# Kernel tuning notes

Hardware: AMD Instinct MI355X
Metric: run time of the kernel (lower is better)

The kernel has to match this reference:

```python
import jax, jax.numpy as jnp
import numpy as np


def _glorot(key, shape):
    fan_in, fan_out = shape[0], shape[1]
    lim = np.sqrt(6.0 / (fan_in + fan_out))
    return jax.random.uniform(key, shape, jnp.float32, -lim, lim)


def setup_inputs() -> dict:
    key = jax.random.key(0)
    ks = jax.random.split(key, 32)
    B, NR, NT = 16384, 64, 128
    inp = {
        "tier0_features": jax.random.normal(ks[0], (B, 44), jnp.float32),
        "robot_features": jax.random.normal(ks[1], (B, NR, 6), jnp.float32),
        "track_features": jax.random.normal(ks[2], (B, NT, 7), jnp.float32),
        # robot SetEncoder: 6 -> 64 -> 64 -> 32
        "rw1": _glorot(ks[3], (6, 64)),  "rb1": jnp.zeros((64,), jnp.float32),
        "rw2": _glorot(ks[4], (64, 64)), "rb2": jnp.zeros((64,), jnp.float32),
        "rw3": _glorot(ks[5], (64, 32)), "rb3": jnp.zeros((32,), jnp.float32),
        # track SetEncoder: 7 -> 64 -> 64 -> 32
        "tw1": _glorot(ks[6], (7, 64)),  "tb1": jnp.zeros((64,), jnp.float32),
        "tw2": _glorot(ks[7], (64, 64)), "tb2": jnp.zeros((64,), jnp.float32),
        "tw3": _glorot(ks[8], (64, 32)), "tb3": jnp.zeros((32,), jnp.float32),
        # head MLP: 108 -> 128 -> 128 -> 64 -> 1
        "mw1": _glorot(ks[9], (108, 128)),  "mb1": jnp.zeros((128,), jnp.float32),
        "mw2": _glorot(ks[10], (128, 128)), "mb2": jnp.zeros((128,), jnp.float32),
        "mw3": _glorot(ks[11], (128, 64)),  "mb3": jnp.zeros((64,), jnp.float32),
        "mw4": _glorot(ks[12], (64, 1)),    "mb4": jnp.zeros((1,), jnp.float32),
    }
    return inp


def _set_encode(x, w1, b1, w2, b2, w3, b3):
    # x: [B, N, d_in] -> pooled [B, 32]; mask=None path: mean+max over set dim
    h = jax.nn.relu(jnp.einsum('bnd,dh->bnh', x, w1) + b1)
    h = jax.nn.relu(jnp.einsum('bnh,hk->bnk', h, w2) + b2)
    e = jnp.einsum('bnk,ko->bno', h, w3) + b3
    return (e.mean(axis=1) + e.max(axis=1)) * 0.5


def reference(tier0_features, robot_features, track_features,
              rw1, rb1, rw2, rb2, rw3, rb3,
              tw1, tb1, tw2, tb2, tw3, tb3,
              mw1, mb1, mw2, mb2, mw3, mb3, mw4, mb4):
    robot_emb = _set_encode(robot_features, rw1, rb1, rw2, rb2, rw3, rb3)  # [B,32]
    track_emb = _set_encode(track_features, tw1, tb1, tw2, tb2, tw3, tb3)  # [B,32]
    c = jnp.concatenate([tier0_features, robot_emb, track_emb], axis=1)    # [B,108]
    h = jax.nn.relu(c @ mw1 + mb1)
    h = jax.nn.relu(h @ mw2 + mb2)
    h = jax.nn.relu(h @ mw3 + mb3)
    return (h @ mw4 + mb4).squeeze(-1)  # [B]
```

## Files before the change

### kernel.cpp

```cpp
#include <hip/hip_runtime.h>
#include <hip/hip_bf16.h>

#define DEV_INLINE __device__ __forceinline__
#define MEM_FENCE asm volatile("" ::: "memory")

typedef __bf16 bf16x8 __attribute__((ext_vector_type(8)));
typedef float  floatx4 __attribute__((ext_vector_type(4)));

DEV_INLINE bf16x8 ld_frag(const __bf16* p) {
    union { uint4 u; bf16x8 v; } t;
    t.u = *(const uint4*)p;
    return t.v;
}
DEV_INLINE bf16x8 pack_relu2(floatx4 a, floatx4 b) {
    float2 p0 = {fmaxf(a[0], 0.0f), fmaxf(a[1], 0.0f)};
    float2 p1 = {fmaxf(a[2], 0.0f), fmaxf(a[3], 0.0f)};
    float2 p2 = {fmaxf(b[0], 0.0f), fmaxf(b[1], 0.0f)};
    float2 p3 = {fmaxf(b[2], 0.0f), fmaxf(b[3], 0.0f)};
    union { __hip_bfloat162 h[4]; bf16x8 v; } t;
    t.h[0] = __float22bfloat162_rn(p0);
    t.h[1] = __float22bfloat162_rn(p1);
    t.h[2] = __float22bfloat162_rn(p2);
    t.h[3] = __float22bfloat162_rn(p3);
    return t.v;
}
DEV_INLINE floatx4 vmax4(floatx4 a, floatx4 b) {
    floatx4 r;
#pragma unroll
    for (int i = 0; i < 4; ++i) r[i] = fmaxf(a[i], b[i]);
    return r;
}

template<int N, int Kp, int Ks>
DEV_INLINE void tp(__bf16* dst, const float* __restrict__ src, int idx0, int stride) {
    for (int e = idx0; e < N * Kp; e += stride) {
        int n = e / Kp, k = e - n * Kp;
        dst[e] = (k < Ks) ? (__bf16)src[k * N + n] : (__bf16)0.0f;
    }
}
template<int N, int K>
DEV_INLINE void tp_perm(__bf16* dst, const float* __restrict__ src, int idx0, int stride) {
    for (int e = idx0; e < N * K; e += stride) {
        int n = e / K, kh = e - n * K;
        int qd = (kh >> 3) & 3, kq = kh >> 5, j = kh & 7;
        int c = (2 * kq + (j >> 2)) * 16 + qd * 4 + (j & 3);
        dst[e] = (__bf16)src[c * N + n];
    }
}

__global__ __launch_bounds__(256)
void prep_kernel(const float* __restrict__ rw1, const float* __restrict__ rw2,
                 const float* __restrict__ rw3,
                 const float* __restrict__ tw1, const float* __restrict__ tw2,
                 const float* __restrict__ tw3,
                 const float* __restrict__ mw1, const float* __restrict__ mw2,
                 const float* __restrict__ mw3, __bf16* __restrict__ wb)
{
    int i0 = blockIdx.x * 256 + threadIdx.x;
    int st = gridDim.x * 256;
    tp     < 64,  32,   6>(wb + 0,     rw1, i0, st);
    tp_perm< 64,  64>     (wb + 2048,  rw2, i0, st);
    tp_perm< 32,  64>     (wb + 6144,  rw3, i0, st);
    tp     < 64,  32,   7>(wb + 8192,  tw1, i0, st);
    tp_perm< 64,  64>     (wb + 10240, tw2, i0, st);
    tp_perm< 32,  64>     (wb + 14336, tw3, i0, st);
    tp     <128, 128, 108>(wb + 16384, mw1, i0, st);
    tp_perm<128, 128>     (wb + 32768, mw2, i0, st);
    tp_perm< 64, 128>     (wb + 49152, mw3, i0, st);
}

struct __align__(16) EncSmem {
    float  e3s[64 * 36];
    float  e3m[64 * 36];
    __bf16 w1[64 * 40];
    __bf16 w2[64 * 72];
    __bf16 w3[32 * 72];
    float  bs[160];
};

template<int DIN, int S>
DEV_INLINE void enc_body(EncSmem& sm, const float* __restrict__ X,
                         const __bf16* __restrict__ wenc,
                         const float* __restrict__ b1, const float* __restrict__ b2,
                         const float* __restrict__ b3,
                         __bf16* __restrict__ out, int bid)
{
    constexpr int NB = 128 / S;
    const int tid = threadIdx.x;
    const int w   = tid >> 6;
    const int l64 = tid & 63;
    const int ln  = l64 & 15;
    const int qd  = l64 >> 4;
    float* pool = (float*)sm.w1;

    {
        const uint4* wsrc = (const uint4*)wenc;
        { int i = tid, r = i >> 2, c = i & 3;  *(uint4*)&sm.w1[r * 40 + c * 8] = wsrc[i]; }
        for (int i = tid; i < 512; i += 256) {
            int r = i >> 3, c = i & 7;  *(uint4*)&sm.w2[r * 72 + c * 8] = wsrc[256 + i];
        }
        { int i = tid, r = i >> 3, c = i & 7;  *(uint4*)&sm.w3[r * 72 + c * 8] = wsrc[768 + i]; }
        if (tid < 160)
            sm.bs[tid] = (tid < 64) ? b1[tid]
                       : (tid < 128) ? b2[tid - 64] : b3[tid - 128];
    }
    __syncthreads();

    bf16x8 xb[2];
#pragma unroll
    for (int t = 0; t < 2; ++t) {
        bf16x8 v;
#pragma unroll
        for (int j = 0; j < 8; ++j) v[j] = (__bf16)0.0f;
        if (qd == 0) {
            const int row = (2 * w + t) * 16 + ln;
            const float* xp = X + ((size_t)bid * 128 + row) * DIN;
#pragma unroll
            for (int j = 0; j < DIN; ++j) v[j] = (__bf16)xp[j];
        }
        xb[t] = v;
    }
    floatx4 a1[2][4];
#pragma unroll
    for (int mt = 0; mt < 4; ++mt) {
        bf16x8 af = ld_frag(&sm.w1[(mt * 16 + ln) * 40 + qd * 8]);
        float4 bv = *(const float4*)&sm.bs[mt * 16 + qd * 4];
#pragma unroll
        for (int t = 0; t < 2; ++t) {
            floatx4 acc = (floatx4){bv.x, bv.y, bv.z, bv.w};
            a1[t][mt] = __builtin_amdgcn_mfma_f32_16x16x32_bf16(af, xb[t], acc, 0, 0, 0);
        }
    }
    bf16x8 f1[2][2];
#pragma unroll
    for (int t = 0; t < 2; ++t)
#pragma unroll
        for (int kq = 0; kq < 2; ++kq)
            f1[t][kq] = pack_relu2(a1[t][2 * kq], a1[t][2 * kq + 1]);

    floatx4 a2[2][4];
#pragma unroll
    for (int mt = 0; mt < 4; ++mt) {
        bf16x8 a0 = ld_frag(&sm.w2[(mt * 16 + ln) * 72 + qd * 8]);
        bf16x8 a1f = ld_frag(&sm.w2[(mt * 16 + ln) * 72 + 32 + qd * 8]);
        float4 bv = *(const float4*)&sm.bs[64 + mt * 16 + qd * 4];
#pragma unroll
        for (int t = 0; t < 2; ++t) {
            floatx4 acc = (floatx4){bv.x, bv.y, bv.z, bv.w};
            acc = __builtin_amdgcn_mfma_f32_16x16x32_bf16(a0, f1[t][0], acc, 0, 0, 0);
            acc = __builtin_amdgcn_mfma_f32_16x16x32_bf16(a1f, f1[t][1], acc, 0, 0, 0);
            a2[t][mt] = acc;
        }
    }
    bf16x8 f2[2][2];
#pragma unroll
    for (int t = 0; t < 2; ++t)
#pragma unroll
        for (int kq = 0; kq < 2; ++kq)
            f2[t][kq] = pack_relu2(a2[t][2 * kq], a2[t][2 * kq + 1]);

    floatx4 a3[2][2];
#pragma unroll
    for (int mt = 0; mt < 2; ++mt) {
        bf16x8 a0 = ld_frag(&sm.w3[(mt * 16 + ln) * 72 + qd * 8]);
        bf16x8 a1f = ld_frag(&sm.w3[(mt * 16 + ln) * 72 + 32 + qd * 8]);
        float4 bv = *(const float4*)&sm.bs[128 + mt * 16 + qd * 4];
#pragma unroll
        for (int t = 0; t < 2; ++t) {
            floatx4 acc = (floatx4){bv.x, bv.y, bv.z, bv.w};
            acc = __builtin_amdgcn_mfma_f32_16x16x32_bf16(a0, f2[t][0], acc, 0, 0, 0);
            acc = __builtin_amdgcn_mfma_f32_16x16x32_bf16(a1f, f2[t][1], acc, 0, 0, 0);
            a3[t][mt] = acc;
        }
    }
#pragma unroll
    for (int mt = 0; mt < 2; ++mt) {
        floatx4 s = a3[0][mt] + a3[1][mt];
        floatx4 m = vmax4(a3[0][mt], a3[1][mt]);
        float4 so = {s[0], s[1], s[2], s[3]};
        float4 mo = {m[0], m[1], m[2], m[3]};
        *(float4*)&sm.e3s[(w * 16 + ln) * 36 + mt * 16 + qd * 4] = so;
        *(float4*)&sm.e3m[(w * 16 + ln) * 36 + mt * 16 + qd * 4] = mo;
    }
    __syncthreads();

    {
        constexpr int R = 64 / NB;
        const int o  = tid & 31;
        const int bi = (tid >> 5) % NB;
        const int ch = tid / (32 * NB);
        const int p0 = bi * R + ch * 8;
        float s = 0.0f, m = -3.4e38f;
#pragma unroll
        for (int r = 0; r < 8; ++r) {
            s += sm.e3s[(p0 + r) * 36 + o];
            m = fmaxf(m, sm.e3m[(p0 + r) * 36 + o]);
        }
        pool[tid] = s;
        pool[256 + tid] = m;
    }
    __syncthreads();
    if (tid < NB * 32) {
        constexpr int C = 8 / NB;
        float s = 0.0f, m = -3.4e38f;
#pragma unroll
        for (int c = 0; c < C; ++c) {
            s += pool[tid + c * 32 * NB];
            m = fmaxf(m, pool[256 + tid + c * 32 * NB]);
        }
        size_t b = (size_t)bid * NB + (tid >> 5);
        out[b * 32 + (tid & 31)] = (__bf16)(0.5f * (s * (1.0f / S) + m));
    }
}

__global__ __launch_bounds__(256)
void enc_fused(const float* __restrict__ rX, const float* __restrict__ tX,
               const __bf16* __restrict__ wb,
               const float* __restrict__ rb1, const float* __restrict__ rb2,
               const float* __restrict__ rb3,
               const float* __restrict__ tb1, const float* __restrict__ tb2,
               const float* __restrict__ tb3,
               __bf16* __restrict__ remb, __bf16* __restrict__ temb, int nr)
{
    __shared__ EncSmem sm;
    if ((int)blockIdx.x < nr)
        enc_body<6, 64>(sm, rX, wb, rb1, rb2, rb3, remb, blockIdx.x);
    else
        enc_body<7, 128>(sm, tX, wb + 8192, tb1, tb2, tb3, temb, blockIdx.x - nr);
}

__global__ __launch_bounds__(256)
void head_mfma(const float* __restrict__ t0,
               const __bf16* __restrict__ remb, const __bf16* __restrict__ temb,
               const __bf16* __restrict__ hw1, const float* __restrict__ b1,
               const __bf16* __restrict__ hw2, const float* __restrict__ b2,
               const __bf16* __restrict__ hw3, const float* __restrict__ b3,
               const float* __restrict__ w4, const float* __restrict__ b4,
               float* __restrict__ out)
{
    __shared__ __align__(16) __bf16 cb[64 * 136];

    const int tid = threadIdx.x;
    const int w   = tid >> 6;
    const int l64 = tid & 63;
    const int ln  = l64 & 15;
    const int qd  = l64 >> 4;
    const int g0  = blockIdx.x * 64;

    for (int i = tid; i < 64 * 44; i += 256) {
        int r = i / 44, k = i - r * 44;
        cb[r * 136 + k] = (__bf16)t0[(size_t)(g0 + r) * 44 + k];
    }
    for (int i = tid; i < 64 * 32; i += 256) {
        int r = i >> 5, k = i & 31;
        cb[r * 136 + 44 + k] = remb[(size_t)(g0 + r) * 32 + k];
        cb[r * 136 + 76 + k] = temb[(size_t)(g0 + r) * 32 + k];
    }
    for (int i = tid; i < 64 * 20; i += 256) {
        int r = i / 20, k = i - r * 20;
        cb[r * 136 + 108 + k] = (__bf16)0.0f;
    }
    __syncthreads();

    bf16x8 cf[4];
#pragma unroll
    for (int kq = 0; kq < 4; ++kq)
        cf[kq] = ld_frag(&cb[(w * 16 + ln) * 136 + kq * 32 + qd * 8]);
    floatx4 acc1[8];
#pragma unroll
    for (int mt = 0; mt < 8; ++mt) {
        float4 bv = *(const float4*)&b1[mt * 16 + qd * 4];
        floatx4 acc = (floatx4){bv.x, bv.y, bv.z, bv.w};
#pragma unroll
        for (int kq = 0; kq < 4; ++kq) {
            bf16x8 af = ld_frag(&hw1[(mt * 16 + ln) * 128 + kq * 32 + qd * 8]);
            acc = __builtin_amdgcn_mfma_f32_16x16x32_bf16(af, cf[kq], acc, 0, 0, 0);
        }
        acc1[mt] = acc;
    }
    bf16x8 f1[4];
#pragma unroll
    for (int kq = 0; kq < 4; ++kq)
        f1[kq] = pack_relu2(acc1[2 * kq], acc1[2 * kq + 1]);

    floatx4 acc2[8];
#pragma unroll
    for (int mt = 0; mt < 8; ++mt) {
        float4 bv = *(const float4*)&b2[mt * 16 + qd * 4];
        floatx4 acc = (floatx4){bv.x, bv.y, bv.z, bv.w};
#pragma unroll
        for (int kq = 0; kq < 4; ++kq) {
            bf16x8 af = ld_frag(&hw2[(mt * 16 + ln) * 128 + kq * 32 + qd * 8]);
            acc = __builtin_amdgcn_mfma_f32_16x16x32_bf16(af, f1[kq], acc, 0, 0, 0);
        }
        acc2[mt] = acc;
    }
    bf16x8 f2[4];
#pragma unroll
    for (int kq = 0; kq < 4; ++kq)
        f2[kq] = pack_relu2(acc2[2 * kq], acc2[2 * kq + 1]);

    floatx4 acc3[4];
#pragma unroll
    for (int mt = 0; mt < 4; ++mt) {
        float4 bv = *(const float4*)&b3[mt * 16 + qd * 4];
        floatx4 acc = (floatx4){bv.x, bv.y, bv.z, bv.w};
#pragma unroll
        for (int kq = 0; kq < 4; ++kq) {
            bf16x8 af = ld_frag(&hw3[(mt * 16 + ln) * 128 + kq * 32 + qd * 8]);
            acc = __builtin_amdgcn_mfma_f32_16x16x32_bf16(af, f2[kq], acc, 0, 0, 0);
        }
        acc3[mt] = acc;
    }

    float part = 0.0f;
#pragma unroll
    for (int mt = 0; mt < 4; ++mt) {
        float4 wv = *(const float4*)&w4[mt * 16 + qd * 4];
        part = fmaf(fmaxf(acc3[mt][0], 0.0f), wv.x, part);
        part = fmaf(fmaxf(acc3[mt][1], 0.0f), wv.y, part);
        part = fmaf(fmaxf(acc3[mt][2], 0.0f), wv.z, part);
        part = fmaf(fmaxf(acc3[mt][3], 0.0f), wv.w, part);
    }
    part += __shfl_xor(part, 16);
    part += __shfl_xor(part, 32);
    if (qd == 0)
        out[g0 + w * 16 + ln] = part + b4[0];
}

extern "C" void kernel_launch(void* const* d_in, const int* in_sizes, int n_in,
                              void* d_out, int out_size, void* d_ws, size_t ws_size,
                              hipStream_t stream)
{
    const float* t0  = (const float*)d_in[0];
    const float* rX  = (const float*)d_in[1];
    const float* tX  = (const float*)d_in[2];
    const float* rw1 = (const float*)d_in[3];  const float* rb1 = (const float*)d_in[4];
    const float* rw2 = (const float*)d_in[5];  const float* rb2 = (const float*)d_in[6];
    const float* rw3 = (const float*)d_in[7];  const float* rb3 = (const float*)d_in[8];
    const float* tw1 = (const float*)d_in[9];  const float* tb1 = (const float*)d_in[10];
    const float* tw2 = (const float*)d_in[11]; const float* tb2 = (const float*)d_in[12];
    const float* tw3 = (const float*)d_in[13]; const float* tb3 = (const float*)d_in[14];
    const float* mw1 = (const float*)d_in[15]; const float* mb1 = (const float*)d_in[16];
    const float* mw2 = (const float*)d_in[17]; const float* mb2 = (const float*)d_in[18];
    const float* mw3 = (const float*)d_in[19]; const float* mb3 = (const float*)d_in[20];
    const float* mw4 = (const float*)d_in[21]; const float* mb4 = (const float*)d_in[22];
    float* out = (float*)d_out;

    const int B = 16384;
    __bf16* remb = (__bf16*)d_ws;
    __bf16* temb = (__bf16*)((char*)d_ws + ((size_t)1 << 20));
    __bf16* wb   = (__bf16*)((char*)d_ws + ((size_t)2 << 20));
    const __bf16* mw1b = wb + 16384; const __bf16* mw2b = wb + 32768;
    const __bf16* mw3b = wb + 49152;

    prep_kernel<<<64, 256, 0, stream>>>(rw1, rw2, rw3, tw1, tw2, tw3,
                                        mw1, mw2, mw3, wb);
    const int nr = (B * 64) / 128;
    const int nt = (B * 128) / 128;
    enc_fused<<<nr + nt, 256, 0, stream>>>(rX, tX, wb,
                                           rb1, rb2, rb3, tb1, tb2, tb3,
                                           remb, temb, nr);
    head_mfma<<<B / 64, 256, 0, stream>>>(t0, remb, temb,
                                          mw1b, mb1, mw2b, mb2, mw3b, mb3,
                                          mw4, mb4, out);
}
```

Before: 252.5 us.

## Make encoder persistent with register-resident weight fragments across tiles

The encoder kernel now launches a fixed grid of 768 blocks, each looping over 32 consecutive 128-row tiles. The MFMA weight fragments are loaded once from global memory into registers, and biases once into shared memory, rather than each tile block restaging weights through shared memory. The intent is to remove per-tile weight-staging traffic and block launch overhead. In exchange it adds register pressure (launch bounds set to 3 blocks per SM). The per-tile loop also has no overlap between loading the next tile and computing the current one, which risks exposing load latency at lower occupancy.

```diff
diff --git a/kernel.cpp b/kernel.cpp
--- a/kernel.cpp
+++ b/kernel.cpp
@@ -2,7 +2,6 @@
 #include <hip/hip_bf16.h>
 
 #define DEV_INLINE __device__ __forceinline__
-#define MEM_FENCE asm volatile("" ::: "memory")
 
 typedef __bf16 bf16x8 __attribute__((ext_vector_type(8)));
 typedef float  floatx4 __attribute__((ext_vector_type(4)));
@@ -70,20 +69,20 @@
 }
 
 struct __align__(16) EncSmem {
-    float  e3s[64 * 36];
-    float  e3m[64 * 36];
-    __bf16 w1[64 * 40];
-    __bf16 w2[64 * 72];
-    __bf16 w3[32 * 72];
-    float  bs[160];
+    float e3s[64 * 36];
+    float e3m[64 * 36];
+    float pool[512];
+    float bs[160];
 };
 
-template<int DIN, int S>
-DEV_INLINE void enc_body(EncSmem& sm, const float* __restrict__ X,
-                         const __bf16* __restrict__ wenc,
+template<int DIN, int S, int ITERS>
+DEV_INLINE void enc_loop(EncSmem& sm, const float* __restrict__ X,
+                         const __bf16* __restrict__ w1p,
+                         const __bf16* __restrict__ w2p,
+                         const __bf16* __restrict__ w3p,
                          const float* __restrict__ b1, const float* __restrict__ b2,
                          const float* __restrict__ b3,
-                         __bf16* __restrict__ out, int bid)
+                         __bf16* __restrict__ out, int bid0)
 {
     constexpr int NB = 128 / S;
     const int tid = threadIdx.x;
@@ -91,142 +90,149 @@
     const int l64 = tid & 63;
     const int ln  = l64 & 15;
     const int qd  = l64 >> 4;
-    float* pool = (float*)sm.w1;
-
-    {
-        const uint4* wsrc = (const uint4*)wenc;
-        { int i = tid, r = i >> 2, c = i & 3;  *(uint4*)&sm.w1[r * 40 + c * 8] = wsrc[i]; }
-        for (int i = tid; i < 512; i += 256) {
-            int r = i >> 3, c = i & 7;  *(uint4*)&sm.w2[r * 72 + c * 8] = wsrc[256 + i];
-        }
-        { int i = tid, r = i >> 3, c = i & 7;  *(uint4*)&sm.w3[r * 72 + c * 8] = wsrc[768 + i]; }
-        if (tid < 160)
-            sm.bs[tid] = (tid < 64) ? b1[tid]
-                       : (tid < 128) ? b2[tid - 64] : b3[tid - 128];
-    }
+
+    if (tid < 160)
+        sm.bs[tid] = (tid < 64) ? b1[tid]
+                   : (tid < 128) ? b2[tid - 64] : b3[tid - 128];
+
+    bf16x8 w1f[4], w2f[4][2], w3f[2][2];
+#pragma unroll
+    for (int mt = 0; mt < 4; ++mt)
+        w1f[mt] = ld_frag(&w1p[(mt * 16 + ln) * 32 + qd * 8]);
+#pragma unroll
+    for (int mt = 0; mt < 4; ++mt)
+#pragma unroll
+        for (int kq = 0; kq < 2; ++kq)
+            w2f[mt][kq] = ld_frag(&w2p[(mt * 16 + ln) * 64 + kq * 32 + qd * 8]);
+#pragma unroll
+    for (int mt = 0; mt < 2; ++mt)
+#pragma unroll
+        for (int kq = 0; kq < 2; ++kq)
+            w3f[mt][kq] = ld_frag(&w3p[(mt * 16 + ln) * 64 + kq * 32 + qd * 8]);
     __syncthreads();
 
-    bf16x8 xb[2];
-#pragma unroll
-    for (int t = 0; t < 2; ++t) {
-        bf16x8 v;
-#pragma unroll
-        for (int j = 0; j < 8; ++j) v[j] = (__bf16)0.0f;
-        if (qd == 0) {
-            const int row = (2 * w + t) * 16 + ln;
-            const float* xp = X + ((size_t)bid * 128 + row) * DIN;
-#pragma unroll
-            for (int j = 0; j < DIN; ++j) v[j] = (__bf16)xp[j];
-        }
-        xb[t] = v;
-    }
-    floatx4 a1[2][4];
-#pragma unroll
-    for (int mt = 0; mt < 4; ++mt) {
-        bf16x8 af = ld_frag(&sm.w1[(mt * 16 + ln) * 40 + qd * 8]);
-        float4 bv = *(const float4*)&sm.bs[mt * 16 + qd * 4];
+    for (int it = 0; it < ITERS; ++it) {
+        const int bid = bid0 + it;
+
+        bf16x8 xb[2];
 #pragma unroll
         for (int t = 0; t < 2; ++t) {
-            floatx4 acc = (floatx4){bv.x, bv.y, bv.z, bv.w};
-            a1[t][mt] = __builtin_amdgcn_mfma_f32_16x16x32_bf16(af, xb[t], acc, 0, 0, 0);
-        }
-    }
-    bf16x8 f1[2][2];
-#pragma unroll
-    for (int t = 0; t < 2; ++t)
-#pragma unroll
-        for (int kq = 0; kq < 2; ++kq)
-            f1[t][kq] = pack_relu2(a1[t][2 * kq], a1[t][2 * kq + 1]);
-
-    floatx4 a2[2][4];
-#pragma unroll
-    for (int mt = 0; mt < 4; ++mt) {
-        bf16x8 a0 = ld_frag(&sm.w2[(mt * 16 + ln) * 72 + qd * 8]);
-        bf16x8 a1f = ld_frag(&sm.w2[(mt * 16 + ln) * 72 + 32 + qd * 8]);
-        float4 bv = *(const float4*)&sm.bs[64 + mt * 16 + qd * 4];
-#pragma unroll
-        for (int t = 0; t < 2; ++t) {
-            floatx4 acc = (floatx4){bv.x, bv.y, bv.z, bv.w};
-            acc = __builtin_amdgcn_mfma_f32_16x16x32_bf16(a0, f1[t][0], acc, 0, 0, 0);
-            acc = __builtin_amdgcn_mfma_f32_16x16x32_bf16(a1f, f1[t][1], acc, 0, 0, 0);
-            a2[t][mt] = acc;
-        }
-    }
-    bf16x8 f2[2][2];
-#pragma unroll
-    for (int t = 0; t < 2; ++t)
-#pragma unroll
-        for (int kq = 0; kq < 2; ++kq)
-            f2[t][kq] = pack_relu2(a2[t][2 * kq], a2[t][2 * kq + 1]);
-
-    floatx4 a3[2][2];
-#pragma unroll
-    for (int mt = 0; mt < 2; ++mt) {
-        bf16x8 a0 = ld_frag(&sm.w3[(mt * 16 + ln) * 72 + qd * 8]);
-        bf16x8 a1f = ld_frag(&sm.w3[(mt * 16 + ln) * 72 + 32 + qd * 8]);
-        float4 bv = *(const float4*)&sm.bs[128 + mt * 16 + qd * 4];
-#pragma unroll
-        for (int t = 0; t < 2; ++t) {
-            floatx4 acc = (floatx4){bv.x, bv.y, bv.z, bv.w};
-            acc = __builtin_amdgcn_mfma_f32_16x16x32_bf16(a0, f2[t][0], acc, 0, 0, 0);
-            acc = __builtin_amdgcn_mfma_f32_16x16x32_bf16(a1f, f2[t][1], acc, 0, 0, 0);
-            a3[t][mt] = acc;
-        }
-    }
-#pragma unroll
-    for (int mt = 0; mt < 2; ++mt) {
-        floatx4 s = a3[0][mt] + a3[1][mt];
-        floatx4 m = vmax4(a3[0][mt], a3[1][mt]);
-        float4 so = {s[0], s[1], s[2], s[3]};
-        float4 mo = {m[0], m[1], m[2], m[3]};
-        *(float4*)&sm.e3s[(w * 16 + ln) * 36 + mt * 16 + qd * 4] = so;
-        *(float4*)&sm.e3m[(w * 16 + ln) * 36 + mt * 16 + qd * 4] = mo;
-    }
-    __syncthreads();
-
-    {
-        constexpr int R = 64 / NB;
-        const int o  = tid & 31;
-        const int bi = (tid >> 5) % NB;
-        const int ch = tid / (32 * NB);
-        const int p0 = bi * R + ch * 8;
-        float s = 0.0f, m = -3.4e38f;
-#pragma unroll
-        for (int r = 0; r < 8; ++r) {
-            s += sm.e3s[(p0 + r) * 36 + o];
-            m = fmaxf(m, sm.e3m[(p0 + r) * 36 + o]);
-        }
-        pool[tid] = s;
-        pool[256 + tid] = m;
-    }
-    __syncthreads();
-    if (tid < NB * 32) {
-        constexpr int C = 8 / NB;
-        float s = 0.0f, m = -3.4e38f;
-#pragma unroll
-        for (int c = 0; c < C; ++c) {
-            s += pool[tid + c * 32 * NB];
-            m = fmaxf(m, pool[256 + tid + c * 32 * NB]);
-        }
-        size_t b = (size_t)bid * NB + (tid >> 5);
-        out[b * 32 + (tid & 31)] = (__bf16)(0.5f * (s * (1.0f / S) + m));
-    }
-}
-
-__global__ __launch_bounds__(256)
+            bf16x8 v;
+#pragma unroll
+            for (int j = 0; j < 8; ++j) v[j] = (__bf16)0.0f;
+            if (qd == 0) {
+                const int row = (2 * w + t) * 16 + ln;
+                const float* xp = X + ((size_t)bid * 128 + row) * DIN;
+#pragma unroll
+                for (int j = 0; j < DIN; ++j) v[j] = (__bf16)xp[j];
+            }
+            xb[t] = v;
+        }
+        floatx4 a1[2][4];
+#pragma unroll
+        for (int mt = 0; mt < 4; ++mt) {
+            float4 bv = *(const float4*)&sm.bs[mt * 16 + qd * 4];
+#pragma unroll
+            for (int t = 0; t < 2; ++t) {
+                floatx4 acc = (floatx4){bv.x, bv.y, bv.z, bv.w};
+                a1[t][mt] = __builtin_amdgcn_mfma_f32_16x16x32_bf16(w1f[mt], xb[t], acc, 0, 0, 0);
+            }
+        }
+        bf16x8 f1[2][2];
+#pragma unroll
+        for (int t = 0; t < 2; ++t)
+#pragma unroll
+            for (int kq = 0; kq < 2; ++kq)
+                f1[t][kq] = pack_relu2(a1[t][2 * kq], a1[t][2 * kq + 1]);
+
+        floatx4 a2[2][4];
+#pragma unroll
+        for (int mt = 0; mt < 4; ++mt) {
+            float4 bv = *(const float4*)&sm.bs[64 + mt * 16 + qd * 4];
+#pragma unroll
+            for (int t = 0; t < 2; ++t) {
+                floatx4 acc = (floatx4){bv.x, bv.y, bv.z, bv.w};
+                acc = __builtin_amdgcn_mfma_f32_16x16x32_bf16(w2f[mt][0], f1[t][0], acc, 0, 0, 0);
+                acc = __builtin_amdgcn_mfma_f32_16x16x32_bf16(w2f[mt][1], f1[t][1], acc, 0, 0, 0);
+                a2[t][mt] = acc;
+            }
+        }
+        bf16x8 f2[2][2];
+#pragma unroll
+        for (int t = 0; t < 2; ++t)
+#pragma unroll
+            for (int kq = 0; kq < 2; ++kq)
+                f2[t][kq] = pack_relu2(a2[t][2 * kq], a2[t][2 * kq + 1]);
+
+        floatx4 a3[2][2];
+#pragma unroll
+        for (int mt = 0; mt < 2; ++mt) {
+            float4 bv = *(const float4*)&sm.bs[128 + mt * 16 + qd * 4];
+#pragma unroll
+            for (int t = 0; t < 2; ++t) {
+                floatx4 acc = (floatx4){bv.x, bv.y, bv.z, bv.w};
+                acc = __builtin_amdgcn_mfma_f32_16x16x32_bf16(w3f[mt][0], f2[t][0], acc, 0, 0, 0);
+                acc = __builtin_amdgcn_mfma_f32_16x16x32_bf16(w3f[mt][1], f2[t][1], acc, 0, 0, 0);
+                a3[t][mt] = acc;
+            }
+        }
+#pragma unroll
+        for (int mt = 0; mt < 2; ++mt) {
+            floatx4 s = a3[0][mt] + a3[1][mt];
+            floatx4 m = vmax4(a3[0][mt], a3[1][mt]);
+            float4 so = {s[0], s[1], s[2], s[3]};
+            float4 mo = {m[0], m[1], m[2], m[3]};
+            *(float4*)&sm.e3s[(w * 16 + ln) * 36 + mt * 16 + qd * 4] = so;
+            *(float4*)&sm.e3m[(w * 16 + ln) * 36 + mt * 16 + qd * 4] = mo;
+        }
+        __syncthreads();
+
+        {
+            constexpr int R = 64 / NB;
+            const int o  = tid & 31;
+            const int bi = (tid >> 5) % NB;
+            const int ch = tid / (32 * NB);
+            const int p0 = bi * R + ch * 8;
+            float s = 0.0f, m = -3.4e38f;
+#pragma unroll
+            for (int r = 0; r < 8; ++r) {
+                s += sm.e3s[(p0 + r) * 36 + o];
+                m = fmaxf(m, sm.e3m[(p0 + r) * 36 + o]);
+            }
+            sm.pool[tid] = s;
+            sm.pool[256 + tid] = m;
+        }
+        __syncthreads();
+        if (tid < NB * 32) {
+            constexpr int C = 8 / NB;
+            float s = 0.0f, m = -3.4e38f;
+#pragma unroll
+            for (int c = 0; c < C; ++c) {
+                s += sm.pool[tid + c * 32 * NB];
+                m = fmaxf(m, sm.pool[256 + tid + c * 32 * NB]);
+            }
+            size_t b = (size_t)bid * NB + (tid >> 5);
+            out[b * 32 + (tid & 31)] = (__bf16)(0.5f * (s * (1.0f / S) + m));
+        }
+    }
+}
+
+__global__ __launch_bounds__(256, 3)
 void enc_fused(const float* __restrict__ rX, const float* __restrict__ tX,
                const __bf16* __restrict__ wb,
                const float* __restrict__ rb1, const float* __restrict__ rb2,
                const float* __restrict__ rb3,
                const float* __restrict__ tb1, const float* __restrict__ tb2,
                const float* __restrict__ tb3,
-               __bf16* __restrict__ remb, __bf16* __restrict__ temb, int nr)
+               __bf16* __restrict__ remb, __bf16* __restrict__ temb)
 {
     __shared__ EncSmem sm;
-    if ((int)blockIdx.x < nr)
-        enc_body<6, 64>(sm, rX, wb, rb1, rb2, rb3, remb, blockIdx.x);
+    if ((int)blockIdx.x < 256)
+        enc_loop<6, 64, 32>(sm, rX, wb, wb + 2048, wb + 6144,
+                            rb1, rb2, rb3, remb, blockIdx.x * 32);
     else
-        enc_body<7, 128>(sm, tX, wb + 8192, tb1, tb2, tb3, temb, blockIdx.x - nr);
+        enc_loop<7, 128, 32>(sm, tX, wb + 8192, wb + 10240, wb + 14336,
+                             tb1, tb2, tb3, temb, (blockIdx.x - 256) * 32);
 }
 
 __global__ __launch_bounds__(256)
@@ -356,11 +362,9 @@
 
     prep_kernel<<<64, 256, 0, stream>>>(rw1, rw2, rw3, tw1, tw2, tw3,
                                         mw1, mw2, mw3, wb);
-    const int nr = (B * 64) / 128;
-    const int nt = (B * 128) / 128;
-    enc_fused<<<nr + nt, 256, 0, stream>>>(rX, tX, wb,
-                                           rb1, rb2, rb3, tb1, tb2, tb3,
-                                           remb, temb, nr);
+    enc_fused<<<768, 256, 0, stream>>>(rX, tX, wb,
+                                       rb1, rb2, rb3, tb1, tb2, tb3,
+                                       remb, temb);
     head_mfma<<<B / 64, 256, 0, stream>>>(t0, remb, temb,
                                           mw1b, mb1, mw2b, mb2, mw3b, mb3,
                                           mw4, mb4, out);
```

Result: faster. 238.6 us (-5.5%).
